# Kernel optimization log

Hardware: AMD Instinct MI355X
Metric: run time of the kernel (lower is better)

## Reference

```python
import jax, jax.numpy as jnp
import numpy as np

NUM_HEADS = 16


def setup_inputs() -> dict:
    key = jax.random.key(0)
    ks = jax.random.split(key, 9)
    B, Nq, Nk = 2, 2048, 2048
    qd, kd, vd = 1024, 1024, 1024
    s = 0.02
    return {
        "query": jax.random.normal(ks[0], (B, Nq, qd), jnp.float32),
        "key": jax.random.normal(ks[1], (B, Nk, kd), jnp.float32),
        "value": jax.random.normal(ks[2], (B, Nk, vd), jnp.float32),
        "Wq": jax.random.normal(ks[3], (qd, qd), jnp.float32) * s,
        "bq": jnp.zeros((qd,), jnp.float32),
        "Wk": jax.random.normal(ks[4], (kd, qd), jnp.float32) * s,
        "bk": jnp.zeros((qd,), jnp.float32),
        "Wv": jax.random.normal(ks[5], (vd, vd), jnp.float32) * s,
        "bv": jnp.zeros((vd,), jnp.float32),
    }


def _split_heads(x, num_heads):
    B, N, D = x.shape
    return x.reshape(B, N, num_heads, D // num_heads).transpose(0, 2, 1, 3)  # [B,H,N,depth]


def reference(query, key, value, Wq, bq, Wk, bk, Wv, bv):
    H = NUM_HEADS
    q = _split_heads(query @ Wq + bq, H)   # [B,H,Nq,dq]
    k = _split_heads(key @ Wk + bk, H)     # [B,H,Nk,dq]
    v = _split_heads(value @ Wv + bv, H)   # [B,H,Nk,dv]
    q_depth = q.shape[-1]
    scores = jnp.einsum('bhqd,bhkd->bhqk', q, k) / jnp.sqrt(jnp.float32(q_depth))
    scores = scores - jnp.max(scores, axis=-1, keepdims=True)
    attn = jax.nn.softmax(scores, axis=-1)  # [B,H,Nq,Nk]
    context = jnp.einsum('bhqk,bhkd->bhqd', attn, v)
    B, _, Nq, dv = context.shape
    context = context.transpose(0, 2, 1, 3).reshape(B, Nq, H * dv)
    return (context, attn)
```

## Files before the change

kernel.cpp:

```cpp
#include <hip/hip_runtime.h>
#include <hip/hip_bf16.h>
#include <stdint.h>

typedef __attribute__((ext_vector_type(4))) float floatx4;
typedef __attribute__((ext_vector_type(8))) short shortx8;

#define NTOK 2048
#define DMODEL 1024
#define NHEAD 16
#define DHEAD 64
#define BATCH 2

static __device__ __forceinline__ unsigned short f2bf(float f) {
    union { float f; unsigned int u; } v; v.f = f;
    return (unsigned short)((v.u + 0x7FFFu + ((v.u >> 16) & 1u)) >> 16);
}

static __device__ __forceinline__ floatx4 mfma16(shortx8 a, shortx8 b, floatx4 c) {
    return __builtin_amdgcn_mfma_f32_16x16x32_bf16(a, b, c, 0, 0, 0);
}

static __device__ __forceinline__ void gl_lds16(const unsigned short* g, unsigned short* l) {
    __builtin_amdgcn_global_load_lds(
        (const __attribute__((address_space(1))) unsigned int*)g,
        (__attribute__((address_space(3))) unsigned int*)l, 16, 0, 0);
}

#define C1 0.18033688f

__global__ void cast_x_kernel(const float* __restrict__ q, const float* __restrict__ k,
                              const float* __restrict__ v,
                              unsigned short* __restrict__ oq, unsigned short* __restrict__ ok,
                              unsigned short* __restrict__ ov) {
    const float* src = blockIdx.y == 0 ? q : (blockIdx.y == 1 ? k : v);
    unsigned short* dst = blockIdx.y == 0 ? oq : (blockIdx.y == 1 ? ok : ov);
    int i = (blockIdx.x * 256 + threadIdx.x) * 8;
    floatx4 a = *(const floatx4*)(src + i);
    floatx4 b = *(const floatx4*)(src + i + 4);
    union { shortx8 s; unsigned short u[8]; } o;
    o.u[0] = f2bf(a[0]); o.u[1] = f2bf(a[1]); o.u[2] = f2bf(a[2]); o.u[3] = f2bf(a[3]);
    o.u[4] = f2bf(b[0]); o.u[5] = f2bf(b[1]); o.u[6] = f2bf(b[2]); o.u[7] = f2bf(b[3]);
    *(shortx8*)(dst + i) = o.s;
}

__global__ void transpose_w_kernel(const float* __restrict__ wq, const float* __restrict__ wk,
                                   const float* __restrict__ wv,
                                   unsigned short* __restrict__ tq, unsigned short* __restrict__ tk,
                                   unsigned short* __restrict__ tv) {
    __shared__ float tile[32][33];
    const float* W = blockIdx.z == 0 ? wq : (blockIdx.z == 1 ? wk : wv);
    unsigned short* T = blockIdx.z == 0 ? tq : (blockIdx.z == 1 ? tk : tv);
    int tx = threadIdx.x, ty = threadIdx.y;
    int bx = blockIdx.x, by = blockIdx.y;
#pragma unroll
    for (int j = 0; j < 4; j++)
        tile[ty + j * 8][tx] = W[(by * 32 + ty + j * 8) * DMODEL + bx * 32 + tx];
    __syncthreads();
#pragma unroll
    for (int j = 0; j < 4; j++)
        T[(bx * 32 + ty + j * 8) * DMODEL + by * 32 + tx] = f2bf(tile[tx][ty + j * 8]);
}

__launch_bounds__(256)
__global__ void proj_gemm_kernel(const unsigned short* __restrict__ xq, const unsigned short* __restrict__ xk,
                                 const unsigned short* __restrict__ xv,
                                 const unsigned short* __restrict__ tq, const unsigned short* __restrict__ tk,
                                 const unsigned short* __restrict__ tv,
                                 const float* __restrict__ bq, const float* __restrict__ bk,
                                 const float* __restrict__ bv,
                                 unsigned short* __restrict__ qh, unsigned short* __restrict__ kh,
                                 unsigned short* __restrict__ vt) {
    int z = blockIdx.z;
    const unsigned short* X = z == 0 ? xq : (z == 1 ? xk : xv);
    const unsigned short* W = z == 0 ? tq : (z == 1 ? tk : tv);
    const float* bias = z == 0 ? bq : (z == 1 ? bk : bv);

    __shared__ unsigned short As[128 * 32];
    __shared__ unsigned short Bs[128 * 32];

    int t = threadIdx.x;
    int lane = t & 63, w = t >> 6;
    int wr = w >> 1, wc = w & 1;
    int r = lane & 15, g = lane >> 4;
    int m0 = blockIdx.y * 128, n0 = blockIdx.x * 128;

    floatx4 acc[4][4];
#pragma unroll
    for (int i = 0; i < 4; i++)
#pragma unroll
        for (int j = 0; j < 4; j++) acc[i][j] = (floatx4){0.f, 0.f, 0.f, 0.f};

    for (int kt = 0; kt < DMODEL; kt += 32) {
#pragma unroll
        for (int i = 0; i < 2; i++) {
            int idx = t + 256 * i;
            int row = idx >> 2, c8 = (idx & 3) * 8;
            gl_lds16(X + (size_t)(m0 + row) * DMODEL + kt + c8, As + idx * 8);
            gl_lds16(W + (size_t)(n0 + row) * DMODEL + kt + c8, Bs + idx * 8);
        }
        __syncthreads();
        shortx8 a[4], b[4];
#pragma unroll
        for (int f = 0; f < 4; f++) {
            a[f] = *(const shortx8*)(As + (wr * 64 + f * 16 + r) * 32 + g * 8);
            b[f] = *(const shortx8*)(Bs + (wc * 64 + f * 16 + r) * 32 + g * 8);
        }
#pragma unroll
        for (int fm = 0; fm < 4; fm++)
#pragma unroll
            for (int fn = 0; fn < 4; fn++)
                acc[fm][fn] = mfma16(a[fm], b[fn], acc[fm][fn]);
        __syncthreads();
    }

    unsigned short* dstQK = (z == 0) ? qh : kh;
#pragma unroll
    for (int fm = 0; fm < 4; fm++) {
#pragma unroll
        for (int fn = 0; fn < 4; fn++) {
            int n = n0 + wc * 64 + fn * 16 + r;
            float bval = bias[n];
            int h = n >> 6, d = n & 63;
#pragma unroll
            for (int reg = 0; reg < 4; reg++) {
                int m = m0 + wr * 64 + fm * 16 + g * 4 + reg;
                int bb = m >> 11, tok = m & 2047;
                unsigned short o = f2bf(acc[fm][fn][reg] + bval);
                if (z < 2)
                    dstQK[(((size_t)(bb * NHEAD + h) * NTOK + tok) * DHEAD) + d] = o;
                else
                    vt[(((size_t)(bb * NHEAD + h) * DHEAD + d) * NTOK) + tok] = o;
            }
        }
    }
}

__launch_bounds__(256, 4)
__global__ void attn_fused_kernel(const unsigned short* __restrict__ Qh,
                                  const unsigned short* __restrict__ Kh,
                                  const unsigned short* __restrict__ Vt,
                                  float* __restrict__ ctx, float* __restrict__ attn) {
    __shared__ __align__(16) unsigned short Kst[2][4096];
    __shared__ __align__(16) unsigned short Aux[2][4096];

    int t = threadIdx.x, lane = t & 63, w = t >> 6, r = lane & 15, g = lane >> 4;

    int bid = blockIdx.y * 64 + blockIdx.x;
    int xcd = bid & 7;
    int j = bid >> 3;
    int bh = xcd * 4 + (j & 3);
    int rest = j >> 2;
    int qb = rest >> 1;
    int role = rest & 1;

    int q0 = qb * 64 + w * 16;
    int qrow = q0 + r;
    int rs = r & 7;

    const unsigned short* Qp = Qh + ((size_t)bh * NTOK + q0) * DHEAD;
    const unsigned short* Kbase = Kh + (size_t)bh * NTOK * DHEAD;
    const unsigned short* Vbase = Vt + (size_t)bh * DHEAD * NTOK;

    shortx8 qf0 = *(const shortx8*)(Qp + r * DHEAD + g * 8);
    shortx8 qf1 = *(const shortx8*)(Qp + r * DHEAD + 32 + g * 8);

    const floatx4 zero = (floatx4){0.f, 0.f, 0.f, 0.f};

    auto STK = [&](int b, int it) {
#pragma unroll
        for (int p = 0; p < 2; ++p) {
            int row = p * 32 + (t >> 3);
            int cb = (t & 7) ^ ((t >> 3) & 7);
            gl_lds16(Kbase + ((size_t)(it * 64 + row)) * DHEAD + cb * 8,
                     Kst[b] + p * 2048 + t * 8);
        }
    };
    auto STV = [&](int b, int it) {
#pragma unroll
        for (int p = 0; p < 2; ++p) {
            int row = p * 32 + (t >> 3);
            int cb = (t & 7) ^ ((t >> 3) & 7);
            gl_lds16(Vbase + (size_t)row * NTOK + it * 64 + cb * 8,
                     Aux[b] + p * 2048 + t * 8);
        }
    };
    auto KF = [&](int b, int tq, int h) -> shortx8 {
        return *(const shortx8*)(Kst[b] + (tq * 16 + r) * 64 + 8 * (((h * 4) + g) ^ rs));
    };
    auto VF = [&](int b, int dt, int h4) -> shortx8 {
        return *(const shortx8*)(Aux[b] + (dt * 16 + r) * 64 + 8 * ((h4 + g) ^ rs));
    };

    if (role == 0) {
        floatx4 pv0 = zero, pv1 = zero, pv2 = zero, pv3 = zero;
        float sm = 0.f;
        const bool hi = (g >= 2);
        const int srcA = (r + ((g & 1) << 5)) << 2;
        const int srcB = srcA + 64;

        STK(0, 0); STV(0, 0);
        __syncthreads();
        for (int it = 0; it < 32; ++it) {
            int cur = it & 1, nxt = cur ^ 1;
            if (it < 31) { STK(nxt, it + 1); STV(nxt, it + 1); }
#pragma unroll
            for (int half = 0; half < 2; ++half) {
                unsigned int p01t0, p23t0, p01t1, p23t1;
                {
                    floatx4 sc = mfma16(KF(cur, half * 2, 0), qf0, zero);
                    sc = mfma16(KF(cur, half * 2, 1), qf1, sc);
                    float e0 = exp2f(C1 * sc[0]), e1 = exp2f(C1 * sc[1]);
                    float e2 = exp2f(C1 * sc[2]), e3 = exp2f(C1 * sc[3]);
                    sm += (e0 + e1) + (e2 + e3);
                    asm("v_cvt_pk_bf16_f32 %0, %1, %2" : "=v"(p01t0) : "v"(e0), "v"(e1));
                    asm("v_cvt_pk_bf16_f32 %0, %1, %2" : "=v"(p23t0) : "v"(e2), "v"(e3));
                }
                {
                    floatx4 sc = mfma16(KF(cur, half * 2 + 1, 0), qf0, zero);
                    sc = mfma16(KF(cur, half * 2 + 1, 1), qf1, sc);
                    float e0 = exp2f(C1 * sc[0]), e1 = exp2f(C1 * sc[1]);
                    float e2 = exp2f(C1 * sc[2]), e3 = exp2f(C1 * sc[3]);
                    sm += (e0 + e1) + (e2 + e3);
                    asm("v_cvt_pk_bf16_f32 %0, %1, %2" : "=v"(p01t1) : "v"(e0), "v"(e1));
                    asm("v_cvt_pk_bf16_f32 %0, %1, %2" : "=v"(p23t1) : "v"(e2), "v"(e3));
                }
                int b0a = __builtin_amdgcn_ds_bpermute(srcA, (int)p01t0);
                int b0b = __builtin_amdgcn_ds_bpermute(srcA, (int)p01t1);
                int b1a = __builtin_amdgcn_ds_bpermute(srcA, (int)p23t0);
                int b1b = __builtin_amdgcn_ds_bpermute(srcA, (int)p23t1);
                int b2a = __builtin_amdgcn_ds_bpermute(srcB, (int)p01t0);
                int b2b = __builtin_amdgcn_ds_bpermute(srcB, (int)p01t1);
                int b3a = __builtin_amdgcn_ds_bpermute(srcB, (int)p23t0);
                int b3b = __builtin_amdgcn_ds_bpermute(srcB, (int)p23t1);
                union { unsigned int u[4]; shortx8 s8; } pbu;
                pbu.u[0] = (unsigned)(hi ? b0b : b0a);
                pbu.u[1] = (unsigned)(hi ? b1b : b1a);
                pbu.u[2] = (unsigned)(hi ? b2b : b2a);
                pbu.u[3] = (unsigned)(hi ? b3b : b3a);
                pv0 = mfma16(VF(cur, 0, half * 4), pbu.s8, pv0);
                pv1 = mfma16(VF(cur, 1, half * 4), pbu.s8, pv1);
                pv2 = mfma16(VF(cur, 2, half * 4), pbu.s8, pv2);
                pv3 = mfma16(VF(cur, 3, half * 4), pbu.s8, pv3);
            }
            __syncthreads();
        }
        float tot = sm;
        tot += __shfl_xor(tot, 16, 64);
        tot += __shfl_xor(tot, 32, 64);
        float inv = 1.0f / tot;
        float* ctx_row =
            ctx + ((size_t)((bh >> 4) * NTOK + qrow)) * DMODEL + (bh & 15) * DHEAD + g * 4;
        *(floatx4*)(ctx_row) = pv0 * inv;
        *(floatx4*)(ctx_row + 16) = pv1 * inv;
        *(floatx4*)(ctx_row + 32) = pv2 * inv;
        *(floatx4*)(ctx_row + 48) = pv3 * inv;
    } else {
        float sm = 0.f;
        STK(0, 0);
        __syncthreads();
        for (int it = 0; it < 32; ++it) {
            int cur = it & 1, nxt = cur ^ 1;
            if (it < 31) STK(nxt, it + 1);
#pragma unroll
            for (int tq = 0; tq < 4; ++tq) {
                floatx4 sc = mfma16(KF(cur, tq, 0), qf0, zero);
                sc = mfma16(KF(cur, tq, 1), qf1, sc);
                sm += (exp2f(C1 * sc[0]) + exp2f(C1 * sc[1])) +
                      (exp2f(C1 * sc[2]) + exp2f(C1 * sc[3]));
            }
            __syncthreads();
        }
        float tot = sm;
        tot += __shfl_xor(tot, 16, 64);
        tot += __shfl_xor(tot, 32, 64);
        float nl2s = -__log2f(tot);

        float(*pw)[64] = (float(*)[64])((char*)Aux + (size_t)w * 4096);
        float* attn_base = attn + ((size_t)bh * NTOK + q0) * NTOK;

        STK(0, 0);
        __syncthreads();
        for (int it = 0; it < 32; ++it) {
            int cur = it & 1, nxt = cur ^ 1;
            if (it < 31) STK(nxt, it + 1);
            int kk0 = it * 64;
#pragma unroll
            for (int tq = 0; tq < 4; ++tq) {
                floatx4 sc = mfma16(KF(cur, tq, 0), qf0, zero);
                sc = mfma16(KF(cur, tq, 1), qf1, sc);
                float e0 = exp2f(fmaf(C1, sc[0], nl2s));
                float e1 = exp2f(fmaf(C1, sc[1], nl2s));
                float e2 = exp2f(fmaf(C1, sc[2], nl2s));
                float e3 = exp2f(fmaf(C1, sc[3], nl2s));
                int x_ = (tq * 4 + g) ^ r;
                *(floatx4*)&pw[r][4 * x_] = (floatx4){e0, e1, e2, e3};
            }
#pragma unroll
            for (int sID = 0; sID < 4; ++sID) {
                int row = 4 * sID + g;
                floatx4 vvv = *(const floatx4*)&pw[row][4 * (r ^ row)];
                __builtin_nontemporal_store(
                    vvv, (floatx4*)(attn_base + (size_t)row * NTOK + kk0 + 4 * r));
            }
            __syncthreads();
        }
    }
}

extern "C" void kernel_launch(void* const* d_in, const int* in_sizes, int n_in,
                              void* d_out, int out_size, void* d_ws, size_t ws_size,
                              hipStream_t stream) {
    const float* query = (const float*)d_in[0];
    const float* key   = (const float*)d_in[1];
    const float* value = (const float*)d_in[2];
    const float* Wq = (const float*)d_in[3];
    const float* bq = (const float*)d_in[4];
    const float* Wk = (const float*)d_in[5];
    const float* bk = (const float*)d_in[6];
    const float* Wv = (const float*)d_in[7];
    const float* bv = (const float*)d_in[8];

    const size_t NX = (size_t)BATCH * NTOK * DMODEL;
    const size_t NW = (size_t)DMODEL * DMODEL;

    unsigned short* ws = (unsigned short*)d_ws;
    unsigned short* Xq = ws;
    unsigned short* Xk = Xq + NX;
    unsigned short* Xv = Xk + NX;
    unsigned short* Tq = Xv + NX;
    unsigned short* Tk = Tq + NW;
    unsigned short* Tv = Tk + NW;
    unsigned short* Qh = Tv + NW;
    unsigned short* Kh = Qh + NX;
    unsigned short* Vt = Kh + NX;

    float* ctx = (float*)d_out;
    float* attn = ctx + NX;

    cast_x_kernel<<<dim3(2048, 3), 256, 0, stream>>>(query, key, value, Xq, Xk, Xv);
    transpose_w_kernel<<<dim3(32, 32, 3), dim3(32, 8), 0, stream>>>(Wq, Wk, Wv, Tq, Tk, Tv);
    proj_gemm_kernel<<<dim3(8, 32, 3), 256, 0, stream>>>(Xq, Xk, Xv, Tq, Tk, Tv,
                                                         bq, bk, bv, Qh, Kh, Vt);
    attn_fused_kernel<<<dim3(64, 32), 256, 0, stream>>>(Qh, Kh, Vt, ctx, attn);
}
```

Baseline: 251.6 us.

## Merge prep kernels, widen projection GEMM K-tile with swizzled LDS and XCD remap

Merges the activation cast and weight transpose into one launch, which saves a kernel launch. The projection GEMM now stages 64-wide K tiles instead of 32, so it needs half as many barriers. It XOR-swizzles the LDS layout to avoid bank conflicts on the fragment reads. It also remaps the linear block ID so neighbouring tiles land on the same XCD, to improve L2 reuse. The larger LDS footprint (32KB per block) may reduce occupancy, and the whole change only touches the projection stage, which is a fraction of total time.

```diff
diff --git a/kernel.cpp b/kernel.cpp
--- a/kernel.cpp
+++ b/kernel.cpp
@@ -28,37 +28,42 @@
 
 #define C1 0.18033688f
 
-__global__ void cast_x_kernel(const float* __restrict__ q, const float* __restrict__ k,
-                              const float* __restrict__ v,
-                              unsigned short* __restrict__ oq, unsigned short* __restrict__ ok,
-                              unsigned short* __restrict__ ov) {
-    const float* src = blockIdx.y == 0 ? q : (blockIdx.y == 1 ? k : v);
-    unsigned short* dst = blockIdx.y == 0 ? oq : (blockIdx.y == 1 ? ok : ov);
-    int i = (blockIdx.x * 256 + threadIdx.x) * 8;
-    floatx4 a = *(const floatx4*)(src + i);
-    floatx4 b = *(const floatx4*)(src + i + 4);
-    union { shortx8 s; unsigned short u[8]; } o;
-    o.u[0] = f2bf(a[0]); o.u[1] = f2bf(a[1]); o.u[2] = f2bf(a[2]); o.u[3] = f2bf(a[3]);
-    o.u[4] = f2bf(b[0]); o.u[5] = f2bf(b[1]); o.u[6] = f2bf(b[2]); o.u[7] = f2bf(b[3]);
-    *(shortx8*)(dst + i) = o.s;
-}
-
-__global__ void transpose_w_kernel(const float* __restrict__ wq, const float* __restrict__ wk,
-                                   const float* __restrict__ wv,
-                                   unsigned short* __restrict__ tq, unsigned short* __restrict__ tk,
-                                   unsigned short* __restrict__ tv) {
+__global__ void prep_kernel(const float* __restrict__ q, const float* __restrict__ k,
+                            const float* __restrict__ v,
+                            const float* __restrict__ wq, const float* __restrict__ wk,
+                            const float* __restrict__ wv,
+                            unsigned short* __restrict__ oq, unsigned short* __restrict__ ok,
+                            unsigned short* __restrict__ ov,
+                            unsigned short* __restrict__ tq, unsigned short* __restrict__ tk,
+                            unsigned short* __restrict__ tv) {
     __shared__ float tile[32][33];
-    const float* W = blockIdx.z == 0 ? wq : (blockIdx.z == 1 ? wk : wv);
-    unsigned short* T = blockIdx.z == 0 ? tq : (blockIdx.z == 1 ? tk : tv);
-    int tx = threadIdx.x, ty = threadIdx.y;
-    int bx = blockIdx.x, by = blockIdx.y;
-#pragma unroll
-    for (int j = 0; j < 4; j++)
-        tile[ty + j * 8][tx] = W[(by * 32 + ty + j * 8) * DMODEL + bx * 32 + tx];
-    __syncthreads();
-#pragma unroll
-    for (int j = 0; j < 4; j++)
-        T[(bx * 32 + ty + j * 8) * DMODEL + by * 32 + tx] = f2bf(tile[tx][ty + j * 8]);
+    int b = blockIdx.x;
+    if (b < 6144) {
+        int part = b >> 11, blk = b & 2047;
+        const float* src = part == 0 ? q : (part == 1 ? k : v);
+        unsigned short* dst = part == 0 ? oq : (part == 1 ? ok : ov);
+        int i = (blk * 256 + threadIdx.x) * 8;
+        floatx4 a = *(const floatx4*)(src + i);
+        floatx4 c = *(const floatx4*)(src + i + 4);
+        union { shortx8 s; unsigned short u[8]; } o;
+        o.u[0] = f2bf(a[0]); o.u[1] = f2bf(a[1]); o.u[2] = f2bf(a[2]); o.u[3] = f2bf(a[3]);
+        o.u[4] = f2bf(c[0]); o.u[5] = f2bf(c[1]); o.u[6] = f2bf(c[2]); o.u[7] = f2bf(c[3]);
+        *(shortx8*)(dst + i) = o.s;
+    } else {
+        int bb = b - 6144;
+        int z = bb >> 10, rem = bb & 1023;
+        int bx = rem & 31, by = rem >> 5;
+        const float* W = z == 0 ? wq : (z == 1 ? wk : wv);
+        unsigned short* T = z == 0 ? tq : (z == 1 ? tk : tv);
+        int tx = threadIdx.x & 31, ty = threadIdx.x >> 5;
+#pragma unroll
+        for (int j = 0; j < 4; j++)
+            tile[ty + j * 8][tx] = W[(by * 32 + ty + j * 8) * DMODEL + bx * 32 + tx];
+        __syncthreads();
+#pragma unroll
+        for (int j = 0; j < 4; j++)
+            T[(bx * 32 + ty + j * 8) * DMODEL + by * 32 + tx] = f2bf(tile[tx][ty + j * 8]);
+    }
 }
 
 __launch_bounds__(256)
@@ -70,19 +75,22 @@
                                  const float* __restrict__ bv,
                                  unsigned short* __restrict__ qh, unsigned short* __restrict__ kh,
                                  unsigned short* __restrict__ vt) {
-    int z = blockIdx.z;
+    int bid = blockIdx.x;
+    int l = (bid & 7) * 96 + (bid >> 3);
+    int x = l & 7, y = (l >> 3) & 31, z = l >> 8;
+
     const unsigned short* X = z == 0 ? xq : (z == 1 ? xk : xv);
     const unsigned short* W = z == 0 ? tq : (z == 1 ? tk : tv);
     const float* bias = z == 0 ? bq : (z == 1 ? bk : bv);
 
-    __shared__ unsigned short As[128 * 32];
-    __shared__ unsigned short Bs[128 * 32];
+    __shared__ unsigned short As[128 * 64];
+    __shared__ unsigned short Bs[128 * 64];
 
     int t = threadIdx.x;
     int lane = t & 63, w = t >> 6;
     int wr = w >> 1, wc = w & 1;
     int r = lane & 15, g = lane >> 4;
-    int m0 = blockIdx.y * 128, n0 = blockIdx.x * 128;
+    int m0 = y * 128, n0 = x * 128;
 
     floatx4 acc[4][4];
 #pragma unroll
@@ -90,26 +98,32 @@
 #pragma unroll
         for (int j = 0; j < 4; j++) acc[i][j] = (floatx4){0.f, 0.f, 0.f, 0.f};
 
-    for (int kt = 0; kt < DMODEL; kt += 32) {
-#pragma unroll
-        for (int i = 0; i < 2; i++) {
+    for (int kt = 0; kt < DMODEL; kt += 64) {
+#pragma unroll
+        for (int i = 0; i < 4; i++) {
             int idx = t + 256 * i;
-            int row = idx >> 2, c8 = (idx & 3) * 8;
-            gl_lds16(X + (size_t)(m0 + row) * DMODEL + kt + c8, As + idx * 8);
-            gl_lds16(W + (size_t)(n0 + row) * DMODEL + kt + c8, Bs + idx * 8);
-        }
-        __syncthreads();
-        shortx8 a[4], b[4];
-#pragma unroll
-        for (int f = 0; f < 4; f++) {
-            a[f] = *(const shortx8*)(As + (wr * 64 + f * 16 + r) * 32 + g * 8);
-            b[f] = *(const shortx8*)(Bs + (wc * 64 + f * 16 + r) * 32 + g * 8);
-        }
-#pragma unroll
-        for (int fm = 0; fm < 4; fm++)
-#pragma unroll
-            for (int fn = 0; fn < 4; fn++)
-                acc[fm][fn] = mfma16(a[fm], b[fn], acc[fm][fn]);
+            int row = idx >> 3;
+            int scb = (idx & 7) ^ (row & 7);
+            gl_lds16(X + (size_t)(m0 + row) * DMODEL + kt + scb * 8, As + idx * 8);
+            gl_lds16(W + (size_t)(n0 + row) * DMODEL + kt + scb * 8, Bs + idx * 8);
+        }
+        __syncthreads();
+#pragma unroll
+        for (int kh = 0; kh < 2; kh++) {
+            shortx8 a[4], b[4];
+#pragma unroll
+            for (int f = 0; f < 4; f++) {
+                int arow = wr * 64 + f * 16 + r;
+                a[f] = *(const shortx8*)(As + arow * 64 + ((kh * 4 + g) ^ (arow & 7)) * 8);
+                int brow = wc * 64 + f * 16 + r;
+                b[f] = *(const shortx8*)(Bs + brow * 64 + ((kh * 4 + g) ^ (brow & 7)) * 8);
+            }
+#pragma unroll
+            for (int fm = 0; fm < 4; fm++)
+#pragma unroll
+                for (int fn = 0; fn < 4; fn++)
+                    acc[fm][fn] = mfma16(a[fm], b[fn], acc[fm][fn]);
+        }
         __syncthreads();
     }
 
@@ -337,9 +351,9 @@
     float* ctx = (float*)d_out;
     float* attn = ctx + NX;
 
-    cast_x_kernel<<<dim3(2048, 3), 256, 0, stream>>>(query, key, value, Xq, Xk, Xv);
-    transpose_w_kernel<<<dim3(32, 32, 3), dim3(32, 8), 0, stream>>>(Wq, Wk, Wv, Tq, Tk, Tv);
-    proj_gemm_kernel<<<dim3(8, 32, 3), 256, 0, stream>>>(Xq, Xk, Xv, Tq, Tk, Tv,
-                                                         bq, bk, bv, Qh, Kh, Vt);
+    prep_kernel<<<dim3(9216), 256, 0, stream>>>(query, key, value, Wq, Wk, Wv,
+                                                Xq, Xk, Xv, Tq, Tk, Tv);
+    proj_gemm_kernel<<<dim3(768), 256, 0, stream>>>(Xq, Xk, Xv, Tq, Tk, Tv,
+                                                    bq, bk, bv, Qh, Kh, Vt);
     attn_fused_kernel<<<dim3(64, 32), 256, 0, stream>>>(Qh, Kh, Vt, ctx, attn);
 }
```

Measured after the change: 260.6 us. 3.6% more time.
